# Kernel tuning notes

Hardware: AMD Instinct MI355X
Metric: run time of the kernel (lower is better)

The kernel has to match this reference:

```python
import jax, jax.numpy as jnp
import numpy as np

H = 512   # hidden_dim
B = 1024  # batch
D = 256   # history length


def setup_inputs() -> dict:
    key = jax.random.key(0)
    k1, k2, k3, k4, k5, k6 = jax.random.split(key, 6)
    return {
        "h_tilde": jax.random.normal(k1, (B, H), dtype=jnp.float32),
        "c_t": jax.random.normal(k2, (B, H), dtype=jnp.float32),
        "h_history": jax.random.normal(k3, (B, D, H), dtype=jnp.float32),
        # learned parameters (nn.Linear stores weight as [out, in]; y = x @ W.T)
        "Waq": jax.random.normal(k4, (H, 2 * H), dtype=jnp.float32) * (1.0 / np.sqrt(2 * H)),
        "Wah": jax.random.normal(k5, (H, H), dtype=jnp.float32) * (1.0 / np.sqrt(H)),
        "ba": jnp.zeros((H,), dtype=jnp.float32),
        "v_t": jax.random.normal(k6, (H,), dtype=jnp.float32),
    }


def reference(h_tilde, c_t, h_history, Waq, Wah, ba, v_t):
    # q_t = [h_tilde ; c_t] -> [B, 2H]; project to [B, H]
    q_t = jnp.concatenate([h_tilde, c_t], axis=1)
    q_proj = q_t @ Waq.T                         # [B, H]
    h_proj = jnp.einsum('bdh,gh->bdg', h_history, Wah)  # [B, D, H]
    # broadcast add + tanh: the large [B, D, H] intermediate
    score_pre = jnp.tanh(q_proj[:, None, :] + h_proj + ba)
    alpha_unscaled = jnp.einsum('bdh,h->bd', score_pre, v_t)  # [B, D]
    alpha = jax.nn.softmax(alpha_unscaled, axis=1)            # [B, D]
    e_t = jnp.einsum('bd,bdh->bh', alpha, h_history)          # [B, H]
    return (e_t, alpha)
```

## Files before the change

kernel.cpp:

```cpp
#include <hip/hip_runtime.h>
#include <hip/hip_bf16.h>

#define HDIM 512
#define BDIM 1024
#define DDIM 256
#define MTOT (BDIM * DDIM)

typedef _Float16 half8 __attribute__((ext_vector_type(8)));
typedef float f32x4 __attribute__((ext_vector_type(4)));

__device__ __forceinline__ float ftanh(float x) {
    float e = __expf(2.0f * x);
    return 1.0f - 2.0f / (e + 1.0f);
}

__device__ __forceinline__ void gl_lds16(const _Float16* src, _Float16* dst) {
    __builtin_amdgcn_global_load_lds((const __attribute__((address_space(1))) void*)src,
                                     (__attribute__((address_space(3))) void*)dst,
                                     16, 0, 0);
}

__global__ __launch_bounds__(256) void k_convertW(const float* __restrict__ Wah,
                                                  _Float16* __restrict__ W16) {
    int n = blockIdx.x * 256 + threadIdx.x;
    int chunk = n >> 10, r = n & 1023;
    int kb = r >> 6, kp = (r >> 4) & 3, g = r & 15;
    const float* src = Wah + (size_t)(chunk * 16 + g) * 512 + kb * 32 + kp * 8;
    float4 v0 = *(const float4*)src;
    float4 v1 = *(const float4*)(src + 4);
    half8 h;
    h[0] = (_Float16)v0.x; h[1] = (_Float16)v0.y; h[2] = (_Float16)v0.z; h[3] = (_Float16)v0.w;
    h[4] = (_Float16)v1.x; h[5] = (_Float16)v1.y; h[6] = (_Float16)v1.z; h[7] = (_Float16)v1.w;
    *(half8*)&W16[(size_t)n * 8] = h;
}

__global__ __launch_bounds__(256) void k_qproj(const float* __restrict__ h_tilde,
                                               const float* __restrict__ c_t,
                                               const float* __restrict__ Waq,
                                               const float* __restrict__ ba,
                                               float* __restrict__ qb) {
    __shared__ float qs[4][1024];
    int t = threadIdx.x;
    int b0 = blockIdx.x * 4;
    #pragma unroll
    for (int p = 0; p < 4; p++) {
        int f4 = t + p * 256;
        int e = f4 * 4;
        int row = e >> 10, k = e & 1023;
        float4 v;
        if (k < 512) v = *(const float4*)&h_tilde[(b0 + row) * 512 + k];
        else         v = *(const float4*)&c_t[(b0 + row) * 512 + k - 512];
        *(float4*)&qs[row][k] = v;
    }
    __syncthreads();
    int g0 = t, g1 = t + 256;
    float acc0[4] = {0.f, 0.f, 0.f, 0.f};
    float acc1[4] = {0.f, 0.f, 0.f, 0.f};
    const float4* w0p = (const float4*)&Waq[(size_t)g0 * 1024];
    const float4* w1p = (const float4*)&Waq[(size_t)g1 * 1024];
    #pragma unroll 4
    for (int k4 = 0; k4 < 256; k4++) {
        float4 w0 = w0p[k4];
        float4 w1 = w1p[k4];
        #pragma unroll
        for (int bb = 0; bb < 4; bb++) {
            float4 q = *(const float4*)&qs[bb][k4 * 4];
            acc0[bb] += q.x * w0.x + q.y * w0.y + q.z * w0.z + q.w * w0.w;
            acc1[bb] += q.x * w1.x + q.y * w1.y + q.z * w1.z + q.w * w1.w;
        }
    }
    #pragma unroll
    for (int bb = 0; bb < 4; bb++) {
        qb[(b0 + bb) * 512 + g0] = acc0[bb] + ba[g0];
        qb[(b0 + bb) * 512 + g1] = acc1[bb] + ba[g1];
    }
}

__global__ __launch_bounds__(256, 4) void k_logits(const float* __restrict__ hist,
                                                   const float* __restrict__ qb,
                                                   const _Float16* __restrict__ W16,
                                                   const float* __restrict__ v_t,
                                                   float* __restrict__ logits,
                                                   float* __restrict__ eparts,
                                                   float* __restrict__ ms) {
    __shared__ _Float16 Wb[2][8192];
    __shared__ float qbs[512];
    __shared__ float vsh[512];
    __shared__ float lsh[64];

    int t = threadIdx.x;
    int w = t >> 6, lane = t & 63, l15 = lane & 15, l4 = lane >> 4;
    int bx = blockIdx.x;
    size_t m_base = (size_t)bx * 64;
    int b = bx >> 2;

    qbs[t] = qb[b * 512 + t];
    qbs[t + 256] = qb[b * 512 + 256 + t];
    vsh[t] = v_t[t];
    vsh[t + 256] = v_t[256 + t];

    #pragma unroll
    for (int sg = 0; sg < 4; sg++)
        gl_lds16(W16 + ((size_t)(w * 4 + sg) * 64 + lane) * 8,
                 &Wb[0][(w * 4 + sg) * 512]);

    half8 afr[16];
    const float* xb = hist + (m_base + w * 16 + l15) * 512 + l4 * 8;
    #pragma unroll
    for (int kb = 0; kb < 16; kb++) {
        const float* p = xb + kb * 32;
        float4 v0 = *(const float4*)p;
        float4 v1 = *(const float4*)(p + 4);
        half8 h;
        h[0] = (_Float16)v0.x; h[1] = (_Float16)v0.y; h[2] = (_Float16)v0.z; h[3] = (_Float16)v0.w;
        h[4] = (_Float16)v1.x; h[5] = (_Float16)v1.y; h[6] = (_Float16)v1.z; h[7] = (_Float16)v1.w;
        afr[kb] = h;
    }

    float S[4] = {0.f, 0.f, 0.f, 0.f};

    __syncthreads();

    const _Float16* bufbase0 = &Wb[0][lane * 8];
    const _Float16* bufbase1 = &Wb[1][lane * 8];

    for (int c = 0; c < 32; c++) {
        int cur = c & 1;
        if (c < 31) {
            const _Float16* wc = W16 + (size_t)(c + 1) * 8192;
            _Float16* wd = Wb[cur ^ 1];
            #pragma unroll
            for (int sg = 0; sg < 4; sg++)
                gl_lds16(wc + ((size_t)(w * 4 + sg) * 64 + lane) * 8,
                         &wd[(w * 4 + sg) * 512]);
        }
        const _Float16* bufp = cur ? bufbase1 : bufbase0;
        f32x4 tac = (f32x4){0.f, 0.f, 0.f, 0.f};
        __builtin_amdgcn_s_setprio(1);
        #pragma unroll
        for (int kb = 0; kb < 16; kb++) {
            half8 bf = *(const half8*)(bufp + kb * 512);
            tac = __builtin_amdgcn_mfma_f32_16x16x32_f16(afr[kb], bf, tac, 0, 0, 0);
        }
        __builtin_amdgcn_s_setprio(0);
        float qv = qbs[c * 16 + l15];
        float vv = vsh[c * 16 + l15];
        #pragma unroll
        for (int j = 0; j < 4; j++)
            S[j] += ftanh(tac[j] + qv) * vv;
        __syncthreads();
    }

    #pragma unroll
    for (int j = 0; j < 4; j++) {
        float s = S[j];
        s += __shfl_xor(s, 1, 64);
        s += __shfl_xor(s, 2, 64);
        s += __shfl_xor(s, 4, 64);
        s += __shfl_xor(s, 8, 64);
        if (l15 == 0) {
            logits[m_base + w * 16 + l4 * 4 + j] = s;
            lsh[w * 16 + l4 * 4 + j] = s;
        }
    }
    __syncthreads();

    float lv = lsh[lane];
    float mb = lv;
    mb = fmaxf(mb, __shfl_xor(mb, 1, 64));
    mb = fmaxf(mb, __shfl_xor(mb, 2, 64));
    mb = fmaxf(mb, __shfl_xor(mb, 4, 64));
    mb = fmaxf(mb, __shfl_xor(mb, 8, 64));
    mb = fmaxf(mb, __shfl_xor(mb, 16, 64));
    mb = fmaxf(mb, __shfl_xor(mb, 32, 64));
    float eb = __expf(lv - mb);
    float sb = eb;
    sb += __shfl_xor(sb, 1, 64);
    sb += __shfl_xor(sb, 2, 64);
    sb += __shfl_xor(sb, 4, 64);
    sb += __shfl_xor(sb, 8, 64);
    sb += __shfl_xor(sb, 16, 64);
    sb += __shfl_xor(sb, 32, 64);

    float coef = __expf(lsh[w * 16 + l15] - mb);
    float* ews = (float*)Wb;
    #pragma unroll
    for (int kb = 0; kb < 16; kb++) {
        float ep[8];
        half8 x = afr[kb];
        #pragma unroll
        for (int e2 = 0; e2 < 8; e2++) ep[e2] = coef * (float)x[e2];
        #pragma unroll
        for (int e2 = 0; e2 < 8; e2++) {
            ep[e2] += __shfl_xor(ep[e2], 1, 64);
            ep[e2] += __shfl_xor(ep[e2], 2, 64);
            ep[e2] += __shfl_xor(ep[e2], 4, 64);
            ep[e2] += __shfl_xor(ep[e2], 8, 64);
        }
        if (l15 == 0) {
            #pragma unroll
            for (int e2 = 0; e2 < 8; e2++)
                ews[w * 512 + kb * 32 + l4 * 8 + e2] = ep[e2];
        }
    }
    __syncthreads();
    float v0 = ews[t] + ews[512 + t] + ews[1024 + t] + ews[1536 + t];
    float v1 = ews[256 + t] + ews[768 + t] + ews[1280 + t] + ews[1792 + t];
    eparts[(size_t)bx * 512 + t] = v0;
    eparts[(size_t)bx * 512 + 256 + t] = v1;
    if (t == 0) { ms[bx * 2] = mb; ms[bx * 2 + 1] = sb; }
}

__global__ __launch_bounds__(256) void k_comb(const float* __restrict__ logits,
                                              const float* __restrict__ eparts,
                                              const float* __restrict__ ms,
                                              float* __restrict__ out) {
    int b = blockIdx.x, t = threadIdx.x;
    float m0 = ms[(4 * b + 0) * 2], s0 = ms[(4 * b + 0) * 2 + 1];
    float m1 = ms[(4 * b + 1) * 2], s1 = ms[(4 * b + 1) * 2 + 1];
    float m2 = ms[(4 * b + 2) * 2], s2 = ms[(4 * b + 2) * 2 + 1];
    float m3 = ms[(4 * b + 3) * 2], s3 = ms[(4 * b + 3) * 2 + 1];
    float m = fmaxf(fmaxf(m0, m1), fmaxf(m2, m3));
    float w0 = __expf(m0 - m), w1 = __expf(m1 - m);
    float w2 = __expf(m2 - m), w3 = __expf(m3 - m);
    float Sb = w0 * s0 + w1 * s1 + w2 * s2 + w3 * s3;
    float l = logits[b * 256 + t];
    out[BDIM * HDIM + b * 256 + t] = __expf(l - m) / Sb;
    const float* ep = eparts + (size_t)(4 * b) * 512;
    float a0 = w0 * ep[t] + w1 * ep[512 + t] + w2 * ep[1024 + t] + w3 * ep[1536 + t];
    float a1 = w0 * ep[256 + t] + w1 * ep[768 + t] + w2 * ep[1280 + t] + w3 * ep[1792 + t];
    out[b * 512 + t] = a0 / Sb;
    out[b * 512 + 256 + t] = a1 / Sb;
}

extern "C" void kernel_launch(void* const* d_in, const int* in_sizes, int n_in,
                              void* d_out, int out_size, void* d_ws, size_t ws_size,
                              hipStream_t stream) {
    const float* h_tilde = (const float*)d_in[0];
    const float* c_t     = (const float*)d_in[1];
    const float* hist    = (const float*)d_in[2];
    const float* Waq     = (const float*)d_in[3];
    const float* Wah     = (const float*)d_in[4];
    const float* ba      = (const float*)d_in[5];
    const float* v_t     = (const float*)d_in[6];
    float* out = (float*)d_out;

    char* ws = (char*)d_ws;
    float*    qb     = (float*)ws;
    _Float16* W16    = (_Float16*)(ws + (2u << 20));
    float*    logits = (float*)(ws + (3u << 20));
    float*    eparts = (float*)(ws + (4u << 20));
    float*    ms     = (float*)(ws + (12u << 20));

    k_convertW<<<128, 256, 0, stream>>>(Wah, W16);
    k_qproj<<<256, 256, 0, stream>>>(h_tilde, c_t, Waq, ba, qb);
    k_logits<<<4096, 256, 0, stream>>>(hist, qb, W16, v_t, logits, eparts, ms);
    k_comb<<<1024, 256, 0, stream>>>(logits, eparts, ms, out);
}
```

Measured before the change: 391.7 us.

## Merge prep kernels, stagger weight chunk order, pipeline history loads, use rcp tanh

Merges the weight conversion and query projection into one launch, with extra blocks doing the fp16 weight conversion. In the logits kernel, each block now starts its weight-chunk loop at an offset, so concurrent blocks read different W16 chunks and spread L2/LDS traffic. History loads are software-pipelined through a 4-slot register ring, and tanh uses a raw v_rcp_f32 instead of a division. Together these cut launch overhead, memory contention and ALU cost, at the price of more registers and slightly lower tanh precision.

```diff
diff --git a/kernel.cpp b/kernel.cpp
--- a/kernel.cpp
+++ b/kernel.cpp
@@ -11,7 +11,10 @@
 
 __device__ __forceinline__ float ftanh(float x) {
     float e = __expf(2.0f * x);
-    return 1.0f - 2.0f / (e + 1.0f);
+    float d = e + 1.0f;
+    float r;
+    asm("v_rcp_f32 %0, %1" : "=v"(r) : "v"(d));
+    return 1.0f - 2.0f * r;
 }
 
 __device__ __forceinline__ void gl_lds16(const _Float16* src, _Float16* dst) {
@@ -20,27 +23,28 @@
                                      16, 0, 0);
 }
 
-__global__ __launch_bounds__(256) void k_convertW(const float* __restrict__ Wah,
-                                                  _Float16* __restrict__ W16) {
-    int n = blockIdx.x * 256 + threadIdx.x;
-    int chunk = n >> 10, r = n & 1023;
-    int kb = r >> 6, kp = (r >> 4) & 3, g = r & 15;
-    const float* src = Wah + (size_t)(chunk * 16 + g) * 512 + kb * 32 + kp * 8;
-    float4 v0 = *(const float4*)src;
-    float4 v1 = *(const float4*)(src + 4);
-    half8 h;
-    h[0] = (_Float16)v0.x; h[1] = (_Float16)v0.y; h[2] = (_Float16)v0.z; h[3] = (_Float16)v0.w;
-    h[4] = (_Float16)v1.x; h[5] = (_Float16)v1.y; h[6] = (_Float16)v1.z; h[7] = (_Float16)v1.w;
-    *(half8*)&W16[(size_t)n * 8] = h;
-}
-
-__global__ __launch_bounds__(256) void k_qproj(const float* __restrict__ h_tilde,
-                                               const float* __restrict__ c_t,
-                                               const float* __restrict__ Waq,
-                                               const float* __restrict__ ba,
-                                               float* __restrict__ qb) {
+__global__ __launch_bounds__(256) void k_prep(const float* __restrict__ h_tilde,
+                                              const float* __restrict__ c_t,
+                                              const float* __restrict__ Waq,
+                                              const float* __restrict__ ba,
+                                              const float* __restrict__ Wah,
+                                              float* __restrict__ qb,
+                                              _Float16* __restrict__ W16) {
     __shared__ float qs[4][1024];
     int t = threadIdx.x;
+    if (blockIdx.x >= 256) {
+        int n = (blockIdx.x - 256) * 256 + t;
+        int chunk = n >> 10, r = n & 1023;
+        int kb = r >> 6, kp = (r >> 4) & 3, g = r & 15;
+        const float* src = Wah + (size_t)(chunk * 16 + g) * 512 + kb * 32 + kp * 8;
+        float4 v0 = *(const float4*)src;
+        float4 v1 = *(const float4*)(src + 4);
+        half8 h;
+        h[0] = (_Float16)v0.x; h[1] = (_Float16)v0.y; h[2] = (_Float16)v0.z; h[3] = (_Float16)v0.w;
+        h[4] = (_Float16)v1.x; h[5] = (_Float16)v1.y; h[6] = (_Float16)v1.z; h[7] = (_Float16)v1.w;
+        *(half8*)&W16[(size_t)n * 8] = h;
+        return;
+    }
     int b0 = blockIdx.x * 4;
     #pragma unroll
     for (int p = 0; p < 4; p++) {
@@ -93,6 +97,7 @@
     int bx = blockIdx.x;
     size_t m_base = (size_t)bx * 64;
     int b = bx >> 2;
+    int off = ((bx >> 3) & 3) * 8;
 
     qbs[t] = qb[b * 512 + t];
     qbs[t + 256] = qb[b * 512 + 256 + t];
@@ -101,20 +106,32 @@
 
     #pragma unroll
     for (int sg = 0; sg < 4; sg++)
-        gl_lds16(W16 + ((size_t)(w * 4 + sg) * 64 + lane) * 8,
+        gl_lds16(W16 + (size_t)off * 8192 + ((size_t)(w * 4 + sg) * 64 + lane) * 8,
                  &Wb[0][(w * 4 + sg) * 512]);
 
     half8 afr[16];
     const float* xb = hist + (m_base + w * 16 + l15) * 512 + l4 * 8;
-    #pragma unroll
-    for (int kb = 0; kb < 16; kb++) {
-        const float* p = xb + kb * 32;
-        float4 v0 = *(const float4*)p;
-        float4 v1 = *(const float4*)(p + 4);
-        half8 h;
-        h[0] = (_Float16)v0.x; h[1] = (_Float16)v0.y; h[2] = (_Float16)v0.z; h[3] = (_Float16)v0.w;
-        h[4] = (_Float16)v1.x; h[5] = (_Float16)v1.y; h[6] = (_Float16)v1.z; h[7] = (_Float16)v1.w;
-        afr[kb] = h;
+    {
+        float4 xr0[4], xr1[4];
+        #pragma unroll
+        for (int u = 0; u < 4; u++) {
+            xr0[u] = *(const float4*)(xb + u * 32);
+            xr1[u] = *(const float4*)(xb + u * 32 + 4);
+        }
+        #pragma unroll
+        for (int kb = 0; kb < 16; kb++) {
+            const int slot = kb & 3;
+            float4 v0 = xr0[slot];
+            float4 v1 = xr1[slot];
+            if (kb + 4 < 16) {
+                xr0[slot] = *(const float4*)(xb + (kb + 4) * 32);
+                xr1[slot] = *(const float4*)(xb + (kb + 4) * 32 + 4);
+            }
+            half8 h;
+            h[0] = (_Float16)v0.x; h[1] = (_Float16)v0.y; h[2] = (_Float16)v0.z; h[3] = (_Float16)v0.w;
+            h[4] = (_Float16)v1.x; h[5] = (_Float16)v1.y; h[6] = (_Float16)v1.z; h[7] = (_Float16)v1.w;
+            afr[kb] = h;
+        }
     }
 
     float S[4] = {0.f, 0.f, 0.f, 0.f};
@@ -125,15 +142,19 @@
     const _Float16* bufbase1 = &Wb[1][lane * 8];
 
     for (int c = 0; c < 32; c++) {
+        int cc = (c + off) & 31;
         int cur = c & 1;
         if (c < 31) {
-            const _Float16* wc = W16 + (size_t)(c + 1) * 8192;
+            int cn = (cc + 1) & 31;
+            const _Float16* wc = W16 + (size_t)cn * 8192;
             _Float16* wd = Wb[cur ^ 1];
             #pragma unroll
             for (int sg = 0; sg < 4; sg++)
                 gl_lds16(wc + ((size_t)(w * 4 + sg) * 64 + lane) * 8,
                          &wd[(w * 4 + sg) * 512]);
         }
+        float qv = qbs[cc * 16 + l15];
+        float vv = vsh[cc * 16 + l15];
         const _Float16* bufp = cur ? bufbase1 : bufbase0;
         f32x4 tac = (f32x4){0.f, 0.f, 0.f, 0.f};
         __builtin_amdgcn_s_setprio(1);
@@ -143,8 +164,6 @@
             tac = __builtin_amdgcn_mfma_f32_16x16x32_f16(afr[kb], bf, tac, 0, 0, 0);
         }
         __builtin_amdgcn_s_setprio(0);
-        float qv = qbs[c * 16 + l15];
-        float vv = vsh[c * 16 + l15];
         #pragma unroll
         for (int j = 0; j < 4; j++)
             S[j] += ftanh(tac[j] + qv) * vv;
@@ -252,8 +271,7 @@
     float*    eparts = (float*)(ws + (4u << 20));
     float*    ms     = (float*)(ws + (12u << 20));
 
-    k_convertW<<<128, 256, 0, stream>>>(Wah, W16);
-    k_qproj<<<256, 256, 0, stream>>>(h_tilde, c_t, Waq, ba, qb);
+    k_prep<<<384, 256, 0, stream>>>(h_tilde, c_t, Waq, ba, Wah, qb, W16);
     k_logits<<<4096, 256, 0, stream>>>(hist, qb, W16, v_t, logits, eparts, ms);
     k_comb<<<1024, 256, 0, stream>>>(logits, eparts, ms, out);
 }
```

New measurement: 382.9 us. -2.3%, faster.
